# Performance work log

Measured on AMD Instinct MI355X. Metric: run time of the kernel, lower is better.

The kernel has to match this reference:

```python
import jax, jax.numpy as jnp
import numpy as np

NEG = -1e9  # finite stand-in for -inf so grads stay NaN-free
BLANK = 0

def _lse3(a, b, c):
    m = jnp.maximum(jnp.maximum(a, b), c)
    return m + jnp.log(jnp.exp(a - m) + jnp.exp(b - m) + jnp.exp(c - m))

def setup_inputs() -> dict:
    key = jax.random.key(0)
    k1, k2, k3, k4 = jax.random.split(key, 4)
    T, B, C, S = 1024, 128, 256, 128
    logits = jax.random.normal(k1, (T, B, C), dtype=jnp.float32)
    log_probs = jax.nn.log_softmax(logits, axis=-1)  # CTCLoss expects log-probs
    y = jax.random.randint(k2, (B, S), 1, C)                 # labels in [1, C), never blank
    input_lengths = jax.random.randint(k3, (B,), 768, T + 1)  # 768..T
    target_lengths = jax.random.randint(k4, (B,), 64, S + 1)  # 64..S
    return {"log_probs": log_probs, "y": y,
            "input_lengths": input_lengths, "target_lengths": target_lengths}

def _ctc_loss(log_probs, y, input_lengths, target_lengths):
    T, B, C = log_probs.shape
    S = y.shape[1]
    L = 2 * S + 1  # extended label sequence: blank, y1, blank, y2, ..., blank

    ext = jnp.zeros((B, L), dtype=y.dtype).at[:, 1::2].set(y)  # even slots = blank(0)
    pos = jnp.arange(L)
    prev2 = jnp.concatenate([jnp.full((B, 2), BLANK, dtype=ext.dtype), ext[:, :-2]], axis=1)
    allow_skip = (pos[None, :] >= 2) & (ext != BLANK) & (ext != prev2)  # [B, L]

    # init alpha at t=0: only s=0 (blank) and s=1 (first label) reachable
    lp0 = log_probs[0]  # [B, C]
    alpha0 = jnp.full((B, L), NEG, dtype=log_probs.dtype)
    alpha0 = alpha0.at[:, 0].set(lp0[:, BLANK])
    alpha0 = alpha0.at[:, 1].set(jnp.take_along_axis(lp0, ext[:, 1:2], axis=1)[:, 0])

    def step(alpha, xs):
        lp_t, t = xs  # lp_t: [B, C]
        a0 = alpha
        a1 = jnp.concatenate([jnp.full((B, 1), NEG, alpha.dtype), alpha[:, :-1]], axis=1)
        a2 = jnp.concatenate([jnp.full((B, 2), NEG, alpha.dtype), alpha[:, :-2]], axis=1)
        a2 = jnp.where(allow_skip, a2, NEG)
        emit = jnp.take_along_axis(lp_t, ext, axis=1)  # [B, L]
        new = _lse3(a0, a1, a2) + emit
        # freeze alpha for samples whose input has already ended
        new = jnp.where(t < input_lengths[:, None], new, alpha)
        return new, None

    ts = jnp.arange(1, T)
    alpha_T, _ = jax.lax.scan(step, alpha0, (log_probs[1:], ts))

    # final log-likelihood: logsumexp of alpha at positions 2*tl and 2*tl-1
    idx_hi = (2 * target_lengths)[:, None]       # [B,1]
    idx_lo = (2 * target_lengths - 1)[:, None]
    a_hi = jnp.take_along_axis(alpha_T, idx_hi, axis=1)[:, 0]
    a_lo = jnp.take_along_axis(alpha_T, idx_lo, axis=1)[:, 0]
    m = jnp.maximum(a_hi, a_lo)
    ll = m + jnp.log(jnp.exp(a_hi - m) + jnp.exp(a_lo - m))
    loss = -ll  # per-sample negative log-likelihood

    # zero_infinity=True: zero out infeasible (effectively -inf likelihood) samples
    loss = jnp.where(loss < 0.5 * (-NEG), loss, 0.0)

    # reduction='mean': divide each loss by its target length, then batch mean
    return jnp.mean(loss / target_lengths.astype(loss.dtype))

def reference(log_probs, y, input_lengths, target_lengths):
    return _ctc_loss(log_probs, y, input_lengths, target_lengths)
```

## Files before the change

kernel.cpp:

```cpp
#include <hip/hip_runtime.h>


#define CTC_C 256
#define DEP 16

__device__ __forceinline__ double wshr1_f64(double x) {
  int lo = __double2loint(x), hi = __double2hiint(x);
  lo = __builtin_amdgcn_update_dpp(0, lo, 0x138, 0xf, 0xf, true);
  hi = __builtin_amdgcn_update_dpp(0, hi, 0x138, 0xf, 0xf, true);
  return __hiloint2double(hi, lo);
}

template <int CTRL>
__device__ __forceinline__ unsigned dppmax(unsigned v) {
  unsigned t = (unsigned)__builtin_amdgcn_update_dpp(0, (int)v, CTRL, 0xf, 0xf, true);
  return v > t ? v : t;
}

__device__ __forceinline__ void renorm(double& Oa, double& Ob, double& Ea,
                                       double& Eb, double& E128, double& logC) {
  unsigned m =       (unsigned)__double2hiint(Oa);
  unsigned h;
  h = (unsigned)__double2hiint(Ob);   m = m > h ? m : h;
  h = (unsigned)__double2hiint(Ea);   m = m > h ? m : h;
  h = (unsigned)__double2hiint(Eb);   m = m > h ? m : h;
  h = (unsigned)__double2hiint(E128); m = m > h ? m : h;
  m = dppmax<0xB1>(m);
  m = dppmax<0x4E>(m);
  m = dppmax<0x141>(m);
  m = dppmax<0x140>(m);
  unsigned r0 = (unsigned)__builtin_amdgcn_readlane((int)m, 0);
  unsigned r1 = (unsigned)__builtin_amdgcn_readlane((int)m, 16);
  unsigned r2 = (unsigned)__builtin_amdgcn_readlane((int)m, 32);
  unsigned r3 = (unsigned)__builtin_amdgcn_readlane((int)m, 48);
  unsigned m01 = r0 > r1 ? r0 : r1;
  unsigned m23 = r2 > r3 ? r2 : r3;
  unsigned smax = m01 > m23 ? m01 : m23;
  int eb = (int)(smax >> 20);
  double s = __hiloint2double((int)((unsigned)(2045 - eb) << 20), 0);
  Oa *= s; Ob *= s; Ea *= s; Eb *= s; E128 *= s;
  logC += (double)(eb - 1022) * 0.6931471805599453;
}

__global__ __launch_bounds__(64)
void ctc_fwd(const float* __restrict__ lp, const int* __restrict__ y,
             const int* __restrict__ ilen, const int* __restrict__ tlen,
             float* __restrict__ out, int T, int B, int S) {
  const int b = blockIdx.x;
  const int l = threadIdx.x;
  const size_t rowstrideF = (size_t)B * CTC_C;
  const unsigned ROWB = (unsigned)(B * CTC_C * 4);

  const int len = ilen[b];
  const int tl  = tlen[b];

  const int ya = y[(size_t)b * S + 2 * l];
  const int yb = y[(size_t)b * S + 2 * l + 1];
  const int yprev = __shfl_up(yb, 1);
  const bool skipA = (l > 0) && (ya != yprev);
  const bool skipB = (yb != ya);

  const float* row0 = lp + (size_t)b * CTC_C;
  const int y0 = y[(size_t)b * S];
  double Ea = (l == 0) ? (double)__expf(row0[0])  : 0.;
  double Oa = (l == 0) ? (double)__expf(row0[y0]) : 0.;
  double Eb = 0., Ob = 0., E128 = 0., logC = 0.;

  const int fA = b * CTC_C + ya;
  const int fB = b * CTC_C + yb;
  const int fQ = b * CTC_C;

  float rA[DEP], rB[DEP], rQ[DEP];
#pragma unroll
  for (int t = 1; t <= DEP; ++t) {
    const float* r = lp + (size_t)t * rowstrideF;
    rA[t & 15] = r[fA]; rB[t & 15] = r[fB]; rQ[t & 15] = r[fQ];
  }

  const unsigned capR = (unsigned)(T - 1) * ROWB;
  unsigned uoff = (unsigned)(DEP + 1) * ROWB;

#define CTC_STEP(i_)                                                          \
  do {                                                                        \
    const int d = (1 + (i_)) & 15;                                            \
    const double pa = (double)__expf(rA[d]);                                  \
    const double pb = (double)__expf(rB[d]);                                  \
    const double pq = (double)__expf(rQ[d]);                                  \
    {                                                                         \
      const float* rp = (const float*)((const char*)lp + uoff);               \
      rA[d] = rp[fA]; rB[d] = rp[fB]; rQ[d] = rp[fQ];                         \
      unsigned un = uoff + ROWB;                                              \
      uoff = un < capR ? un : capR;                                           \
    }                                                                         \
    const double Opm1 = wshr1_f64(Ob);              \
    const double EaOp = Ea + Opm1;                                            \
    const double EbOa = Eb + Oa;                                              \
    const double tA = skipA ? EaOp : Ea;                                      \
    const double tB = skipB ? EbOa : Eb;                                      \
    const double nOa = (Oa + tA) * pa;                                        \
    const double nOb = (Ob + tB) * pb;                                        \
    Ea = EaOp * pq;                                                           \
    Eb = EbOa * pq;                                                           \
    E128 = (E128 + Ob) * pq;                        \
    Oa = nOa; Ob = nOb;                                                       \
    __builtin_amdgcn_sched_barrier(0);                                        \
  } while (0)

  const int nsteps = len - 1;
  const int nch = nsteps >> 4;
  const int rem = nsteps & 15;

  for (int c = 0; c < nch; ++c) {
#pragma unroll
    for (int i = 0; i < 16; ++i) {
      CTC_STEP(i);
      if ((i & 7) == 7) renorm(Oa, Ob, Ea, Eb, E128, logC);
    }
  }
  if (rem) {
#pragma unroll
    for (int i = 0; i < 16; ++i) {
      if (i < rem) {
        CTC_STEP(i);
        if ((i & 7) == 7) renorm(Oa, Ob, Ea, Eb, E128, logC);
      }
    }
  }
#undef CTC_STEP

  double vEa = __shfl(Ea, (tl >> 1) & 63);
  double vEb = __shfl(Eb, (tl >> 1) & 63);
  double vE128 = __shfl(E128, 63);
  double vhi = (tl == S) ? vE128 : ((tl & 1) ? vEb : vEa);
  const int s2 = tl - 1;
  double vOa = __shfl(Oa, (s2 >> 1) & 63);
  double vOb = __shfl(Ob, (s2 >> 1) & 63);
  double vlo = (s2 & 1) ? vOb : vOa;

  double sum = vhi + vlo;
  double loss;
  if (sum > 0.) {
    loss = -(logC + log(sum));
  } else {
    loss = 1e30;
  }
  if (!(loss < 5.0e8)) loss = 0.;
  float contrib = (float)(loss / (double)tl / (double)B);
  if (l == 0) atomicAdd(out, contrib);
}

extern "C" void kernel_launch(void* const* d_in, const int* in_sizes, int n_in,
                              void* d_out, int out_size, void* d_ws, size_t ws_size,
                              hipStream_t stream) {
  const float* lp   = (const float*)d_in[0];
  const int*   yy   = (const int*)d_in[1];
  const int*   ilen = (const int*)d_in[2];
  const int*   tlen = (const int*)d_in[3];
  float* out = (float*)d_out;

  int B = in_sizes[2];
  int S = in_sizes[1] / B;
  int T = in_sizes[0] / (B * CTC_C);

  hipMemsetAsync(out, 0, sizeof(float), stream);
  ctc_fwd<<<B, 64, 0, stream>>>(lp, yy, ilen, tlen, out, T, B, S);
}
```

Baseline: 258.9 us.

## Stream full log-prob rows into LDS ring via global_load_lds

Replaces per-lane scattered global gathers (three per step, 16-deep register prefetch) with coalesced 16-byte-per-lane global_load_lds copies of each whole 256-float row into a 16-slot LDS ring. Per-step values are then read from LDS two steps ahead, and explicit vmcnt waits control the pipeline depth. This aims to cut the latency and uncoalesced-access cost of random gathers on the serial recurrence path. In exchange it moves a full row per step instead of three floats and depends on hand-tuned waitcnt counts, with no barrier guarding LDS reuse.

```diff
diff --git a/kernel.cpp b/kernel.cpp
--- a/kernel.cpp
+++ b/kernel.cpp
@@ -2,7 +2,16 @@
 
 
 #define CTC_C 256
-#define DEP 16
+#define RING 16
+#define PFD  2
+
+typedef unsigned int u32;
+
+__device__ __forceinline__ void gll16(const void* g, void* l) {
+  __builtin_amdgcn_global_load_lds(
+      (const __attribute__((address_space(1))) u32*)g,
+      (__attribute__((address_space(3))) u32*)l, 16, 0, 0);
+}
 
 __device__ __forceinline__ double wshr1_f64(double x) {
   int lo = __double2loint(x), hi = __double2hiint(x);
@@ -46,9 +55,10 @@
 void ctc_fwd(const float* __restrict__ lp, const int* __restrict__ y,
              const int* __restrict__ ilen, const int* __restrict__ tlen,
              float* __restrict__ out, int T, int B, int S) {
+  __shared__ __align__(16) float ring[RING][CTC_C];
+
   const int b = blockIdx.x;
   const int l = threadIdx.x;
-  const size_t rowstrideF = (size_t)B * CTC_C;
   const unsigned ROWB = (unsigned)(B * CTC_C * 4);
 
   const int len = ilen[b];
@@ -66,32 +76,42 @@
   double Oa = (l == 0) ? (double)__expf(row0[y0]) : 0.;
   double Eb = 0., Ob = 0., E128 = 0., logC = 0.;
 
-  const int fA = b * CTC_C + ya;
-  const int fB = b * CTC_C + yb;
-  const int fQ = b * CTC_C;
+  const char* gLane = (const char*)lp + (size_t)b * CTC_C * 4 + 16 * (size_t)l;
 
-  float rA[DEP], rB[DEP], rQ[DEP];
+  asm volatile("s_waitcnt vmcnt(0)" ::: "memory");
+  __builtin_amdgcn_sched_barrier(0);
+
 #pragma unroll
-  for (int t = 1; t <= DEP; ++t) {
-    const float* r = lp + (size_t)t * rowstrideF;
-    rA[t & 15] = r[fA]; rB[t & 15] = r[fB]; rQ[t & 15] = r[fQ];
-  }
+  for (int t = 1; t <= RING; ++t)
+    gll16(gLane + (size_t)t * ROWB, &ring[t & 15][0]);
+  asm volatile("s_waitcnt vmcnt(0)" ::: "memory");
+  __builtin_amdgcn_sched_barrier(0);
+
+  float pfA[2], pfB[2], pfQ[2];
+  pfA[1] = ring[1][ya]; pfB[1] = ring[1][yb]; pfQ[1] = ring[1][0];
+  pfA[0] = ring[2][ya]; pfB[0] = ring[2][yb]; pfQ[0] = ring[2][0];
 
   const unsigned capR = (unsigned)(T - 1) * ROWB;
-  unsigned uoff = (unsigned)(DEP + 1) * ROWB;
+  unsigned uoff = (unsigned)(RING + 1) * ROWB;
 
 #define CTC_STEP(i_)                                                          \
   do {                                                                        \
-    const int d = (1 + (i_)) & 15;                                            \
-    const double pa = (double)__expf(rA[d]);                                  \
-    const double pb = (double)__expf(rB[d]);                                  \
-    const double pq = (double)__expf(rQ[d]);                                  \
+    const int dp = (1 + (i_)) & 1;                   \
+    const int sl = (3 + (i_)) & 15;                  \
+    const int sg = (1 + (i_)) & 15;                \
+    const double pa = (double)__expf(pfA[dp]);                                \
+    const double pb = (double)__expf(pfB[dp]);                                \
+    const double pq = (double)__expf(pfQ[dp]);                                \
+    gll16(gLane + uoff, &ring[sg][0]);                                        \
     {                                                                         \
-      const float* rp = (const float*)((const char*)lp + uoff);               \
-      rA[d] = rp[fA]; rB[d] = rp[fB]; rQ[d] = rp[fQ];                         \
       unsigned un = uoff + ROWB;                                              \
       uoff = un < capR ? un : capR;                                           \
     }                                                                         \
+    asm volatile("s_waitcnt vmcnt(14)" ::: "memory");                         \
+    __builtin_amdgcn_sched_barrier(0);                                        \
+    pfA[dp] = ring[sl][ya];                                                   \
+    pfB[dp] = ring[sl][yb];                                                   \
+    pfQ[dp] = ring[sl][0];                                                    \
     const double Opm1 = wshr1_f64(Ob);              \
     const double EaOp = Ea + Opm1;                                            \
     const double EbOa = Eb + Oa;                                              \
```

Result: no change. 258.7 us (-0.0%).

## Process two batch samples per wavefront and drop deep prefetch ring

Applied to the files above, without the earlier changes.

Each 64-lane wavefront now runs the CTC alpha recursion for two batch samples at once, interleaving their independent dependency chains so the scheduler can hide latency. The kernel launches B/2 blocks instead of B. The 16-deep register prefetch ring is replaced by a single-step lookahead load. Renormalisation now runs every 16 steps instead of every 8, and its cross-lane max uses two more DPP row broadcasts with one readlane instead of four readlanes. The trade-off is half as many wavefronts for the recursion-bound workload and more memory latency exposed per step, in exchange for instruction-level overlap between the two chains.

```diff
diff --git a/kernel.cpp b/kernel.cpp
--- a/kernel.cpp
+++ b/kernel.cpp
@@ -2,7 +2,6 @@
 
 
 #define CTC_C 256
-#define DEP 16
 
 __device__ __forceinline__ double wshr1_f64(double x) {
   int lo = __double2loint(x), hi = __double2hiint(x);
@@ -29,13 +28,9 @@
   m = dppmax<0x4E>(m);
   m = dppmax<0x141>(m);
   m = dppmax<0x140>(m);
-  unsigned r0 = (unsigned)__builtin_amdgcn_readlane((int)m, 0);
-  unsigned r1 = (unsigned)__builtin_amdgcn_readlane((int)m, 16);
-  unsigned r2 = (unsigned)__builtin_amdgcn_readlane((int)m, 32);
-  unsigned r3 = (unsigned)__builtin_amdgcn_readlane((int)m, 48);
-  unsigned m01 = r0 > r1 ? r0 : r1;
-  unsigned m23 = r2 > r3 ? r2 : r3;
-  unsigned smax = m01 > m23 ? m01 : m23;
+  m = dppmax<0x142>(m);
+  m = dppmax<0x143>(m);
+  unsigned smax = (unsigned)__builtin_amdgcn_readlane((int)m, 63);
   int eb = (int)(smax >> 20);
   double s = __hiloint2double((int)((unsigned)(2045 - eb) << 20), 0);
   Oa *= s; Ob *= s; Ea *= s; Eb *= s; E128 *= s;
@@ -46,107 +41,126 @@
 void ctc_fwd(const float* __restrict__ lp, const int* __restrict__ y,
              const int* __restrict__ ilen, const int* __restrict__ tlen,
              float* __restrict__ out, int T, int B, int S) {
-  const int b = blockIdx.x;
   const int l = threadIdx.x;
-  const size_t rowstrideF = (size_t)B * CTC_C;
   const unsigned ROWB = (unsigned)(B * CTC_C * 4);
 
-  const int len = ilen[b];
-  const int tl  = tlen[b];
+  int n[2], tl2[2];
+  int fA[2], fB[2], fQ[2];
+  bool skA[2], skB[2];
+  double Oa[2], Ob[2], Ea[2], Eb[2], E128[2], logC[2];
+  float cA[2], cB[2], cQ[2];
 
-  const int ya = y[(size_t)b * S + 2 * l];
-  const int yb = y[(size_t)b * S + 2 * l + 1];
-  const int yprev = __shfl_up(yb, 1);
-  const bool skipA = (l > 0) && (ya != yprev);
-  const bool skipB = (yb != ya);
-
-  const float* row0 = lp + (size_t)b * CTC_C;
-  const int y0 = y[(size_t)b * S];
-  double Ea = (l == 0) ? (double)__expf(row0[0])  : 0.;
-  double Oa = (l == 0) ? (double)__expf(row0[y0]) : 0.;
-  double Eb = 0., Ob = 0., E128 = 0., logC = 0.;
-
-  const int fA = b * CTC_C + ya;
-  const int fB = b * CTC_C + yb;
-  const int fQ = b * CTC_C;
-
-  float rA[DEP], rB[DEP], rQ[DEP];
 #pragma unroll
-  for (int t = 1; t <= DEP; ++t) {
-    const float* r = lp + (size_t)t * rowstrideF;
-    rA[t & 15] = r[fA]; rB[t & 15] = r[fB]; rQ[t & 15] = r[fQ];
+  for (int j = 0; j < 2; ++j) {
+    const int b = 2 * (int)blockIdx.x + j;
+    n[j]   = ilen[b] - 1;
+    tl2[j] = tlen[b];
+    const int ya = y[(size_t)b * S + 2 * l];
+    const int yb = y[(size_t)b * S + 2 * l + 1];
+    const int yprev = __shfl_up(yb, 1);
+    skA[j] = (l > 0) && (ya != yprev);
+    skB[j] = (yb != ya);
+    fA[j] = b * CTC_C + ya;
+    fB[j] = b * CTC_C + yb;
+    fQ[j] = b * CTC_C;
+    const float* row0 = lp + (size_t)b * CTC_C;
+    const int y0 = y[(size_t)b * S];
+    Ea[j] = (l == 0) ? (double)__expf(row0[0])  : 0.;
+    Oa[j] = (l == 0) ? (double)__expf(row0[y0]) : 0.;
+    Eb[j] = 0.; Ob[j] = 0.; E128[j] = 0.; logC[j] = 0.;
+    const float* r1 = lp + (size_t)B * CTC_C;
+    cA[j] = r1[fA[j]]; cB[j] = r1[fB[j]]; cQ[j] = r1[fQ[j]];
   }
 
   const unsigned capR = (unsigned)(T - 1) * ROWB;
-  unsigned uoff = (unsigned)(DEP + 1) * ROWB;
+  unsigned uoff = 2u * ROWB;
 
-#define CTC_STEP(i_)                                                          \
-  do {                                                                        \
-    const int d = (1 + (i_)) & 15;                                            \
-    const double pa = (double)__expf(rA[d]);                                  \
-    const double pb = (double)__expf(rB[d]);                                  \
-    const double pq = (double)__expf(rQ[d]);                                  \
-    {                                                                         \
-      const float* rp = (const float*)((const char*)lp + uoff);               \
-      rA[d] = rp[fA]; rB[d] = rp[fB]; rQ[d] = rp[fQ];                         \
-      unsigned un = uoff + ROWB;                                              \
-      uoff = un < capR ? un : capR;                                           \
-    }                                                                         \
-    const double Opm1 = wshr1_f64(Ob);              \
-    const double EaOp = Ea + Opm1;                                            \
-    const double EbOa = Eb + Oa;                                              \
-    const double tA = skipA ? EaOp : Ea;                                      \
-    const double tB = skipB ? EbOa : Eb;                                      \
-    const double nOa = (Oa + tA) * pa;                                        \
-    const double nOb = (Ob + tB) * pb;                                        \
-    Ea = EaOp * pq;                                                           \
-    Eb = EbOa * pq;                                                           \
-    E128 = (E128 + Ob) * pq;                        \
-    Oa = nOa; Ob = nOb;                                                       \
-    __builtin_amdgcn_sched_barrier(0);                                        \
+#define CTC_STEP(act0_, act1_)                                              \
+  do {                                                                      \
+    double pa[2], pb[2], pq[2];                                             \
+    _Pragma("unroll")                                                       \
+    for (int j = 0; j < 2; ++j) {                                           \
+      pa[j] = (double)__expf(cA[j]);                                        \
+      pb[j] = (double)__expf(cB[j]);                                        \
+      pq[j] = (double)__expf(cQ[j]);                                        \
+    }                                                                       \
+    {                                                                       \
+      const float* rp = (const float*)((const char*)lp + uoff);             \
+      _Pragma("unroll")                                                     \
+      for (int j = 0; j < 2; ++j) {                                         \
+        cA[j] = rp[fA[j]];                                                  \
+        cB[j] = rp[fB[j]];                                                  \
+        cQ[j] = rp[fQ[j]];                                                  \
+      }                                                                     \
+      unsigned un = uoff + ROWB;                                            \
+      uoff = un < capR ? un : capR;                                         \
+    }                                                                       \
+    _Pragma("unroll")                                                       \
+    for (int j = 0; j < 2; ++j) {                                           \
+      const double Opm1 = wshr1_f64(Ob[j]);       \
+      const double EaOp = Ea[j] + Opm1;                                     \
+      const double EbOa = Eb[j] + Oa[j];                                    \
+      const double tA = skA[j] ? EaOp : Ea[j];                              \
+      const double tB = skB[j] ? EbOa : Eb[j];                              \
+      const double nOa = (Oa[j] + tA) * pa[j];                              \
+      const double nOb = (Ob[j] + tB) * pb[j];                              \
+      const double nEa = EaOp * pq[j];                                      \
+      const double nEb = EbOa * pq[j];                                      \
+      const double nE  = (E128[j] + Ob[j]) * pq[j];    \
+      const bool act = (j == 0) ? (act0_) : (act1_);                        \
+      if (act) {                                                            \
+        Oa[j] = nOa; Ob[j] = nOb; Ea[j] = nEa; Eb[j] = nEb; E128[j] = nE;   \
+      }                                                                     \
+    }                                                                       \
   } while (0)
 
-  const int nsteps = len - 1;
-  const int nch = nsteps >> 4;
-  const int rem = nsteps & 15;
+  const int nmin = n[0] < n[1] ? n[0] : n[1];
+  const int nmax = n[0] > n[1] ? n[0] : n[1];
+  const int ncomm = nmin >> 4;
 
-  for (int c = 0; c < nch; ++c) {
+  for (int c = 0; c < ncomm; ++c) {
 #pragma unroll
     for (int i = 0; i < 16; ++i) {
-      CTC_STEP(i);
-      if ((i & 7) == 7) renorm(Oa, Ob, Ea, Eb, E128, logC);
+      CTC_STEP(true, true);
+      if (i == 15) {
+        renorm(Oa[0], Ob[0], Ea[0], Eb[0], E128[0], logC[0]);
+        renorm(Oa[1], Ob[1], Ea[1], Eb[1], E128[1], logC[1]);
+      }
     }
   }
-  if (rem) {
-#pragma unroll
-    for (int i = 0; i < 16; ++i) {
-      if (i < rem) {
-        CTC_STEP(i);
-        if ((i & 7) == 7) renorm(Oa, Ob, Ea, Eb, E128, logC);
-      }
+  for (int t = 16 * ncomm + 1; t <= nmax; ++t) {
+    CTC_STEP(t <= n[0], t <= n[1]);
+    if ((t & 15) == 0) {
+      renorm(Oa[0], Ob[0], Ea[0], Eb[0], E128[0], logC[0]);
+      renorm(Oa[1], Ob[1], Ea[1], Eb[1], E128[1], logC[1]);
     }
   }
 #undef CTC_STEP
 
-  double vEa = __shfl(Ea, (tl >> 1) & 63);
-  double vEb = __shfl(Eb, (tl >> 1) & 63);
-  double vE128 = __shfl(E128, 63);
-  double vhi = (tl == S) ? vE128 : ((tl & 1) ? vEb : vEa);
-  const int s2 = tl - 1;
-  double vOa = __shfl(Oa, (s2 >> 1) & 63);
-  double vOb = __shfl(Ob, (s2 >> 1) & 63);
-  double vlo = (s2 & 1) ? vOb : vOa;
+  float acc = 0.f;
+#pragma unroll
+  for (int j = 0; j < 2; ++j) {
+    const int tl = tl2[j];
+    double vEa = __shfl(Ea[j], (tl >> 1) & 63);
+    double vEb = __shfl(Eb[j], (tl >> 1) & 63);
+    double vE128 = __shfl(E128[j], 63);
+    double vhi = (tl == S) ? vE128 : ((tl & 1) ? vEb : vEa);
+    const int s2 = tl - 1;
+    double vOa = __shfl(Oa[j], (s2 >> 1) & 63);
+    double vOb = __shfl(Ob[j], (s2 >> 1) & 63);
+    double vlo = (s2 & 1) ? vOb : vOa;
 
-  double sum = vhi + vlo;
-  double loss;
-  if (sum > 0.) {
-    loss = -(logC + log(sum));
-  } else {
-    loss = 1e30;
+    double sum = vhi + vlo;
+    double loss;
+    if (sum > 0.) {
+      loss = -(logC[j] + log(sum));
+    } else {
+      loss = 1e30;
+    }
+    if (!(loss < 5.0e8)) loss = 0.;
+    acc += (float)(loss / (double)tl / (double)B);
   }
-  if (!(loss < 5.0e8)) loss = 0.;
-  float contrib = (float)(loss / (double)tl / (double)B);
-  if (l == 0) atomicAdd(out, contrib);
+  if (l == 0) atomicAdd(out, acc);
 }
 
 extern "C" void kernel_launch(void* const* d_in, const int* in_sizes, int n_in,
@@ -163,5 +177,5 @@
   int T = in_sizes[0] / (B * CTC_C);
 
   hipMemsetAsync(out, 0, sizeof(float), stream);
-  ctc_fwd<<<B, 64, 0, stream>>>(lp, yy, ilen, tlen, out, T, B, S);
+  ctc_fwd<<<B / 2, 64, 0, stream>>>(lp, yy, ilen, tlen, out, T, B, S);
 }
```

New measurement: 492.5 us. +90.3%, slower.
